# Optimization experiments

Hardware: AMD Instinct MI355X
Metric: run time of the kernel (lower is better)

The kernel has to match this reference:

```python
import jax, jax.numpy as jnp
import numpy as np

H = 2048      # hidden_size
DM = 4096     # intermediate_size
N = 16        # ssm state size
K = 4         # conv kernel
R = 128       # time_step_rank
B_SZ = 1
L = 1024


def setup_inputs() -> dict:
    key = jax.random.key(0)
    ks = jax.random.split(key, 10)
    s = 0.02
    hidden_states = jax.random.normal(ks[0], (B_SZ, L, H), dtype=jnp.float32)
    W_in = jax.random.normal(ks[1], (2 * DM, H), dtype=jnp.float32) * s
    conv_w = jax.random.normal(ks[2], (DM, 1, K), dtype=jnp.float32) * 0.3
    conv_b = jax.random.normal(ks[3], (DM,), dtype=jnp.float32) * 0.1
    W_x = jax.random.normal(ks[4], (R + 2 * N, DM), dtype=jnp.float32) * s
    W_dt = jax.random.normal(ks[5], (DM, R), dtype=jnp.float32) * s
    b_dt = jax.random.normal(ks[6], (DM,), dtype=jnp.float32) * 0.1
    # A_log init: log(arange(1..N)) broadcast over channels (per __init__)
    A_log = jnp.broadcast_to(jnp.log(jnp.arange(1, N + 1, dtype=jnp.float32))[None, :], (DM, N)).copy()
    D_param = jnp.ones((DM,), dtype=jnp.float32)
    W_out = jax.random.normal(ks[7], (H, DM), dtype=jnp.float32) * s
    return {"hidden_states": hidden_states, "W_in": W_in, "conv_w": conv_w,
            "conv_b": conv_b, "W_x": W_x, "W_dt": W_dt, "b_dt": b_dt,
            "A_log": A_log, "D_param": D_param, "W_out": W_out}


def reference(hidden_states, W_in, conv_w, conv_b, W_x, W_dt, b_dt, A_log, D_param, W_out):
    # in_proj then chunk into hidden / gate (torch chunks dim=1 after transpose)
    proj = hidden_states @ W_in.T                     # [B, L, 2D]
    h, gate = proj[..., :DM], proj[..., DM:]          # each [B, L, D]
    # depthwise causal conv1d, padding K-1 then truncate to L (left-pad == same)
    h_cl = jnp.transpose(h, (0, 2, 1))                # [B, D, L]
    hc = jax.lax.conv_general_dilated(
        h_cl, conv_w, window_strides=(1,), padding=[(K - 1, 0)],
        dimension_numbers=("NCH", "OIH", "NCH"), feature_group_count=DM)
    hc = jax.nn.silu(hc + conv_b[None, :, None])      # [B, D, L]
    hc_ld = jnp.transpose(hc, (0, 2, 1))              # [B, L, D]
    # x_proj -> dt, B, C
    ssm_p = hc_ld @ W_x.T                             # [B, L, R+2N]
    ts, Bm, Cm = ssm_p[..., :R], ssm_p[..., R:R + N], ssm_p[..., R + N:]
    dt = jax.nn.softplus(ts @ W_dt.T + b_dt)          # [B, L, D]
    A = -jnp.exp(A_log)                               # [D, N]
    dA = jnp.exp(dt[:, :, :, None] * A[None, None, :, :])            # [B, L, D, N]
    dBu = dt[:, :, :, None] * Bm[:, :, None, :] * hc_ld[:, :, :, None]  # [B, L, D, N]
    # selective scan over time: state = dA*state + dBu; y = <state, C>
    def step(state, inp):
        dA_t, dBu_t, C_t = inp                        # [B,D,N],[B,D,N],[B,N]
        state = dA_t * state + dBu_t
        y = jnp.einsum("bdn,bn->bd", state, C_t)
        return state, y
    init = jnp.zeros((hidden_states.shape[0], DM, N), dtype=hidden_states.dtype)
    _, ys = jax.lax.scan(step, init,
                         (jnp.swapaxes(dA, 0, 1), jnp.swapaxes(dBu, 0, 1), jnp.swapaxes(Cm, 0, 1)))
    y = jnp.transpose(ys, (1, 0, 2))                  # [B, L, D]
    y = y + hc_ld * D_param[None, None, :]            # skip via D
    y = y * jax.nn.silu(gate)                         # gating
    return y @ W_out.T                                # [B, L, H]
```

## Files before the change

kernel.cpp:

```cpp
#include <hip/hip_runtime.h>
#include <math.h>

#define AS1 __attribute__((address_space(1)))
#define AS3 __attribute__((address_space(3)))

typedef __attribute__((ext_vector_type(8))) short short8;
typedef __attribute__((ext_vector_type(4))) float f32x4;

#define WAITV(n) asm volatile("s_waitcnt vmcnt(" #n ")" ::: "memory")
#define BARRIER() asm volatile("s_barrier" ::: "memory")

static __device__ __forceinline__ unsigned short f2bf(float f) {
    unsigned u = __float_as_uint(f);
    unsigned r = (u + 0x7fffu + ((u >> 16) & 1u)) >> 16;
    return (unsigned short)r;
}
static __device__ __forceinline__ float bf2f(unsigned short u) {
    return __uint_as_float(((unsigned)u) << 16);
}

__global__ __launch_bounds__(256) void cvt_f32_bf16(const float* __restrict__ src,
                                                    unsigned short* __restrict__ dst,
                                                    int n4) {
    int i = blockIdx.x * 256 + threadIdx.x;
    int stride = gridDim.x * 256;
    for (; i < n4; i += stride) {
        float4 v = ((const float4*)src)[i];
        ushort4 o;
        o.x = f2bf(v.x); o.y = f2bf(v.y); o.z = f2bf(v.z); o.w = f2bf(v.w);
        ((ushort4*)dst)[i] = o;
    }
}

__global__ __launch_bounds__(256) void cvt_ts(const float* __restrict__ ssmp,
                                              unsigned short* __restrict__ ts) {
    int i = blockIdx.x * 256 + threadIdx.x;
    int t = i >> 5, c4 = (i & 31) * 4;
    float4 v = *(const float4*)&ssmp[t * 160 + c4];
    ushort4 o;
    o.x = f2bf(v.x); o.y = f2bf(v.y); o.z = f2bf(v.z); o.w = f2bf(v.w);
    *(ushort4*)&ts[t * 128 + c4] = o;
}

__global__ __launch_bounds__(256) void conv_silu(const float* __restrict__ h,
                                                 const float* __restrict__ cw,
                                                 const float* __restrict__ cb,
                                                 unsigned short* __restrict__ hc_bf) {
    int idx = blockIdx.x * 256 + threadIdx.x;
    int d = idx & 4095, t = idx >> 12;
    float acc = cb[d];
    float4 w = *(const float4*)&cw[d * 4];
    const float* wp = (const float*)&w;
#pragma unroll
    for (int k = 0; k < 4; ++k) {
        int tt = t + k - 3;
        if (tt >= 0) acc += h[tt * 4096 + d] * wp[k];
    }
    float s = acc / (1.f + __expf(-acc));
    hc_bf[idx] = f2bf(s);
}

__global__ __launch_bounds__(256) void reduce4(const float* __restrict__ pA,
                                               const float* __restrict__ pB,
                                               float* __restrict__ out, int n4) {
    int i = blockIdx.x * 256 + threadIdx.x;
    int stride = gridDim.x * 256;
    const size_t MN4 = (size_t)1024 * 2048 / 4;
    for (; i < n4; i += stride) {
        float4 a = ((const float4*)pA)[i];
        float4 b = ((const float4*)pA)[i + MN4];
        float4 c = ((const float4*)pB)[i];
        float4 d = ((const float4*)pB)[i + MN4];
        float4 o;
        o.x = (a.x + b.x) + (c.x + d.x);
        o.y = (a.y + b.y) + (c.y + d.y);
        o.z = (a.z + b.z) + (c.z + d.z);
        o.w = (a.w + b.w) + (c.w + d.w);
        ((float4*)out)[i] = o;
    }
}

enum { P_GATE = 0, P_PART = 1 };

template <int EPI>
__global__ __launch_bounds__(512, 2)
void gemm8p(const short* __restrict__ A, const short* __restrict__ B,
            void* __restrict__ C0v, void* __restrict__ C1v,
            int N, int K, int kchunk) {
    __shared__ short lds[3 * 24576];

    const int tid = threadIdx.x;
    const int wv = tid >> 6, ln = tid & 63;
    const int lr = ln & 15, kg = ln >> 4;
    const int wm = wv >> 2, wn = wv & 3;

    const int nwg = gridDim.x;
    const int bid = blockIdx.x;
    const int swz = (bid & 7) * (nwg >> 3) + (bid >> 3);
    const int by = swz & 7, bx = swz >> 3;
    const int m0 = by * 128;
    const int n0 = bx * 256;
    const int kbeg = blockIdx.z * kchunk;
    const int NT = kchunk >> 6;

    f32x4 acc[4][4];
#pragma unroll
    for (int mi = 0; mi < 4; ++mi)
#pragma unroll
        for (int ni = 0; ni < 4; ++ni) acc[mi][ni] = (f32x4){0.f, 0.f, 0.f, 0.f};

    const short* Abase = A + (size_t)m0 * K + kbeg;
    const short* Bbase = B + (size_t)n0 * K + kbeg;

#define STAGE(kt, b)                                                          \
    {                                                                         \
        short* lbase = &lds[(b) * 24576];                                     \
        _Pragma("unroll")                                                     \
        for (int r = 0; r < 2; ++r) {                                         \
            int c = r * 512 + tid;                                            \
            int row = c >> 3, cb8 = (c & 7) << 4;                             \
            int scb = cb8 ^ ((row & 7) << 4);                                 \
            const short* src = Abase + (size_t)row * K + (kt) * 64 + (scb >> 1); \
            short* dst = lbase + (r * 512 + wv * 64) * 8;                     \
            __builtin_amdgcn_global_load_lds((const AS1 void*)src,            \
                                             (AS3 void*)dst, 16, 0, 0);       \
        }                                                                     \
        _Pragma("unroll")                                                     \
        for (int r = 0; r < 4; ++r) {                                         \
            int c = r * 512 + tid;                                            \
            int row = c >> 3, cb8 = (c & 7) << 4;                             \
            int scb = cb8 ^ ((row & 7) << 4);                                 \
            const short* src = Bbase + (size_t)row * K + (kt) * 64 + (scb >> 1); \
            short* dst = lbase + 8192 + (r * 512 + wv * 64) * 8;              \
            __builtin_amdgcn_global_load_lds((const AS1 void*)src,            \
                                             (AS3 void*)dst, 16, 0, 0);       \
        }                                                                     \
    }
#define RD_A(dst, mi, ks)                                                     \
    { int row = wm * 64 + (mi) * 16 + lr;                                     \
      int col = ((ks) * 32 + kg * 8) ^ ((row & 7) << 3);                      \
      dst = *(const short8*)&la[row * 64 + col]; }
#define RD_B(dst, ni, ks)                                                     \
    { int row = wn * 64 + (ni) * 16 + lr;                                     \
      int col = ((ks) * 32 + kg * 8) ^ ((row & 7) << 3);                      \
      dst = *(const short8*)&lb[row * 64 + col]; }
#define MFMA4(mi, a)                                                          \
    acc[mi][0] = __builtin_amdgcn_mfma_f32_16x16x32_bf16(a, vb0, acc[mi][0], 0, 0, 0); \
    acc[mi][1] = __builtin_amdgcn_mfma_f32_16x16x32_bf16(a, vb1, acc[mi][1], 0, 0, 0); \
    acc[mi][2] = __builtin_amdgcn_mfma_f32_16x16x32_bf16(a, vb2, acc[mi][2], 0, 0, 0); \
    acc[mi][3] = __builtin_amdgcn_mfma_f32_16x16x32_bf16(a, vb3, acc[mi][3], 0, 0, 0);

    STAGE(0, 0);
    STAGE(1, 1);

    for (int kt = 0; kt < NT; ++kt) {
        const int b = kt % 3;
        if (kt + 1 < NT) { WAITV(6); } else { WAITV(0); }
        BARRIER();
        if (kt + 2 < NT) STAGE(kt + 2, (kt + 2) % 3);

        const short* la = &lds[b * 24576];
        const short* lb = la + 8192;
        short8 va0, va1, va2, va3, vb0, vb1, vb2, vb3;
        RD_B(vb0, 0, 0); RD_B(vb1, 1, 0); RD_B(vb2, 2, 0); RD_B(vb3, 3, 0);
        RD_A(va0, 0, 0); RD_A(va1, 1, 0); RD_A(va2, 2, 0); RD_A(va3, 3, 0);
        __builtin_amdgcn_s_setprio(1);
        MFMA4(0, va0); MFMA4(1, va1); MFMA4(2, va2); MFMA4(3, va3);
        __builtin_amdgcn_s_setprio(0);
        RD_B(vb0, 0, 1); RD_B(vb1, 1, 1); RD_B(vb2, 2, 1); RD_B(vb3, 3, 1);
        RD_A(va0, 0, 1); RD_A(va1, 1, 1); RD_A(va2, 2, 1); RD_A(va3, 3, 1);
        __builtin_amdgcn_s_setprio(1);
        MFMA4(0, va0); MFMA4(1, va1); MFMA4(2, va2); MFMA4(3, va3);
        __builtin_amdgcn_s_setprio(0);
    }
#undef STAGE
#undef RD_A
#undef RD_B
#undef MFMA4

#pragma unroll
    for (int mi = 0; mi < 4; ++mi) {
        int crow0 = m0 + wm * 64 + mi * 16 + kg * 4;
#pragma unroll
        for (int ni = 0; ni < 4; ++ni) {
            int ccol = n0 + wn * 64 + ni * 16 + lr;
#pragma unroll
            for (int i = 0; i < 4; ++i) {
                float v = acc[mi][ni][i];
                size_t crow = (size_t)(crow0 + i);
                if constexpr (EPI == P_GATE) {
                    if (ccol < 4096) ((float*)C0v)[crow * 4096 + ccol] = v;
                    else {
                        float s = v / (1.f + __expf(-v));
                        ((unsigned short*)C1v)[crow * 4096 + (ccol - 4096)] = f2bf(s);
                    }
                } else {
                    float* P = (float*)(blockIdx.z < 2 ? C0v : C1v) +
                               (size_t)(blockIdx.z & 1) * 1024 * 2048;
                    P[crow * N + ccol] = v;
                }
            }
        }
    }
}

enum { EPI_PLAIN = 0, EPI_SPLIT = 1, EPI_ATOMIC = 2, EPI_SOFTPLUS = 3 };

template <int BM, int EPI>
__global__ __launch_bounds__(256)
void gemm_bt(const short* __restrict__ A, const short* __restrict__ B,
             float* __restrict__ C, float* __restrict__ C2,
             const float* __restrict__ bias,
             int M, int N, int K, int ldc, int kcLen) {
    __shared__ short A_lds[BM * 32];
    __shared__ short B_lds[128 * 32];
    const int tid = threadIdx.x;
    const int wv = tid >> 6, ln = tid & 63;
    const int lr = ln & 15, kg = ln >> 4;
    const int m0 = blockIdx.y * BM;
    const int n0 = blockIdx.x * 128;
    const int kbeg = blockIdx.z * kcLen;
    const int kend = kbeg + kcLen;
    const int wm = wv >> 1, wn = wv & 1;
    constexpr int MR = BM / 32;

    f32x4 acc[MR][4];
#pragma unroll
    for (int mi = 0; mi < MR; ++mi)
#pragma unroll
        for (int ni = 0; ni < 4; ++ni) acc[mi][ni] = (f32x4){0.f, 0.f, 0.f, 0.f};

    const int arow = tid >> 2;
    const int kq8 = (tid & 3) * 8;

    for (int k0 = kbeg; k0 < kend; k0 += 32) {
#pragma unroll
        for (int r = 0; r < BM / 64; ++r) {
            const short* srcA = A + (size_t)(m0 + r * 64 + arow) * K + (k0 + kq8);
            short* dstA = &A_lds[(r * 64 + wv * 16) * 32];
            __builtin_amdgcn_global_load_lds((const AS1 void*)srcA, (AS3 void*)dstA, 16, 0, 0);
        }
#pragma unroll
        for (int r = 0; r < 2; ++r) {
            int brow = n0 + r * 64 + arow;
            if (brow > N - 1) brow = N - 1;
            const short* srcB = B + (size_t)brow * K + (k0 + kq8);
            short* dstB = &B_lds[(r * 64 + wv * 16) * 32];
            __builtin_amdgcn_global_load_lds((const AS1 void*)srcB, (AS3 void*)dstB, 16, 0, 0);
        }
        __syncthreads();

        short8 av[MR], bv[4];
#pragma unroll
        for (int mi = 0; mi < MR; ++mi)
            av[mi] = *(const short8*)&A_lds[(wm * (BM / 2) + mi * 16 + lr) * 32 + kg * 8];
#pragma unroll
        for (int ni = 0; ni < 4; ++ni)
            bv[ni] = *(const short8*)&B_lds[(wn * 64 + ni * 16 + lr) * 32 + kg * 8];
#pragma unroll
        for (int mi = 0; mi < MR; ++mi)
#pragma unroll
            for (int ni = 0; ni < 4; ++ni)
                acc[mi][ni] = __builtin_amdgcn_mfma_f32_16x16x32_bf16(av[mi], bv[ni], acc[mi][ni], 0, 0, 0);
        __syncthreads();
    }

#pragma unroll
    for (int mi = 0; mi < MR; ++mi) {
        int crow0 = m0 + wm * (BM / 2) + mi * 16 + kg * 4;
#pragma unroll
        for (int ni = 0; ni < 4; ++ni) {
            int ccol = n0 + wn * 64 + ni * 16 + lr;
#pragma unroll
            for (int i = 0; i < 4; ++i) {
                float v = acc[mi][ni][i];
                size_t crow = (size_t)(crow0 + i);
                if constexpr (EPI == EPI_PLAIN) {
                    C[crow * ldc + ccol] = v;
                } else if constexpr (EPI == EPI_SPLIT) {
                    if (ccol < 4096) C[crow * 4096 + ccol] = v;
                    else C2[crow * 4096 + (ccol - 4096)] = v;
                } else if constexpr (EPI == EPI_ATOMIC) {
                    if (ccol < N) atomicAdd(&C[crow * ldc + ccol], v);
                } else {
                    float x = v + bias[ccol];
                    float sp = fmaxf(x, 0.f) + log1pf(__expf(-fabsf(x)));
                    ((unsigned short*)C)[crow * ldc + ccol] = f2bf(sp);
                }
            }
        }
    }
}

#define CLEN 16
#define NCH 64

__global__ __launch_bounds__(256)
void scan_p1(const unsigned short* __restrict__ dt, const unsigned short* __restrict__ hc,
             const float* __restrict__ ssmp, const float* __restrict__ A_log,
             float* __restrict__ Sbuf, float* __restrict__ dtsum) {
    const int tid = threadIdx.x;
    const int c = blockIdx.x & (NCH - 1);
    const int db = blockIdx.x >> 6;
    const int d = db * 256 + tid;
    const int t0 = c * CLEN;

    float Ac[16];
#pragma unroll
    for (int i = 0; i < 4; ++i) {
        float4 v = *(const float4*)&A_log[d * 16 + i * 4];
        Ac[i*4+0] = -__expf(v.x); Ac[i*4+1] = -__expf(v.y);
        Ac[i*4+2] = -__expf(v.z); Ac[i*4+3] = -__expf(v.w);
    }

    __shared__ float sB[CLEN][16];
    sB[tid >> 4][tid & 15] = ssmp[(t0 + (tid >> 4)) * 160 + 128 + (tid & 15)];
    __syncthreads();

    float st[16];
#pragma unroll
    for (int n = 0; n < 16; ++n) st[n] = 0.f;
    float ds = 0.f;

    for (int tt = 0; tt < CLEN; ++tt) {
        size_t g = (size_t)(t0 + tt) * 4096 + d;
        float dtv = bf2f(dt[g]);
        float hcv = bf2f(hc[g]);
        float du = dtv * hcv;
        ds += dtv;
#pragma unroll
        for (int n = 0; n < 16; ++n) {
            float dA = __expf(dtv * Ac[n]);
            st[n] = fmaf(dA, st[n], du * sB[tt][n]);
        }
    }

    float* o = Sbuf + ((size_t)c * 4096 + d) * 16;
#pragma unroll
    for (int i = 0; i < 4; ++i)
        *(float4*)&o[i * 4] = make_float4(st[i*4], st[i*4+1], st[i*4+2], st[i*4+3]);
    dtsum[c * 4096 + d] = ds;
}

__global__ __launch_bounds__(256)
void scan_p2(const float* __restrict__ A_log, const float* __restrict__ dtsum,
             float* __restrict__ S) {
    const int idx = blockIdx.x * 256 + threadIdx.x;
    const int d = idx >> 4;
    const float Ac = -__expf(A_log[idx]);

    float sl[NCH], Pv[NCH];
#pragma unroll
    for (int c = 0; c < NCH; ++c) sl[c] = S[(size_t)c * 65536 + idx];
#pragma unroll
    for (int c = 0; c < NCH; ++c) Pv[c] = __expf(Ac * dtsum[c * 4096 + d]);

    float s = 0.f;
#pragma unroll
    for (int c = 0; c < NCH; ++c) {
        S[(size_t)c * 65536 + idx] = s;
        s = fmaf(Pv[c], s, sl[c]);
    }
}

__global__ __launch_bounds__(256)
void scan_p3(const unsigned short* __restrict__ dt, const unsigned short* __restrict__ hc,
             const float* __restrict__ ssmp, const float* __restrict__ A_log,
             const float* __restrict__ Dp, const unsigned short* __restrict__ gate,
             const float* __restrict__ Sinit, unsigned short* __restrict__ y_bf) {
    const int tid = threadIdx.x;
    const int c = blockIdx.x & (NCH - 1);
    const int db = blockIdx.x >> 6;
    const int d = db * 256 + tid;
    const int t0 = c * CLEN;

    float Ac[16];
#pragma unroll
    for (int i = 0; i < 4; ++i) {
        float4 v = *(const float4*)&A_log[d * 16 + i * 4];
        Ac[i*4+0] = -__expf(v.x); Ac[i*4+1] = -__expf(v.y);
        Ac[i*4+2] = -__expf(v.z); Ac[i*4+3] = -__expf(v.w);
    }
    const float Dcoef = Dp[d];

    __shared__ float sB[CLEN][16], sC[CLEN][16];
    {
        int tt = tid >> 4, nn = tid & 15;
        sB[tt][nn] = ssmp[(t0 + tt) * 160 + 128 + nn];
        sC[tt][nn] = ssmp[(t0 + tt) * 160 + 144 + nn];
    }
    __syncthreads();

    float st[16];
    {
        const float* si = Sinit + ((size_t)c * 4096 + d) * 16;
#pragma unroll
        for (int i = 0; i < 4; ++i) {
            float4 v = *(const float4*)&si[i * 4];
            st[i*4] = v.x; st[i*4+1] = v.y; st[i*4+2] = v.z; st[i*4+3] = v.w;
        }
    }

    for (int tt = 0; tt < CLEN; ++tt) {
        size_t g = (size_t)(t0 + tt) * 4096 + d;
        float dtv = bf2f(dt[g]);
        float hcv = bf2f(hc[g]);
        float du = dtv * hcv;
        float p[16];
#pragma unroll
        for (int n = 0; n < 16; ++n) {
            float dA = __expf(dtv * Ac[n]);
            st[n] = fmaf(dA, st[n], du * sB[tt][n]);
            p[n] = st[n] * sC[tt][n];
        }
#pragma unroll
        for (int n = 0; n < 8; ++n) p[n] += p[n + 8];
#pragma unroll
        for (int n = 0; n < 4; ++n) p[n] += p[n + 4];
        p[0] += p[2]; p[1] += p[3];
        float csum = p[0] + p[1];
        float gv = bf2f(gate[g]);
        float yv = (csum + hcv * Dcoef) * gv;
        y_bf[g] = f2bf(yv);
    }
}

extern "C" void kernel_launch(void* const* d_in, const int* in_sizes, int n_in,
                              void* d_out, int out_size, void* d_ws, size_t ws_size,
                              hipStream_t stream) {
    (void)in_sizes; (void)n_in; (void)out_size; (void)ws_size;
    const float* hidden = (const float*)d_in[0];
    const float* W_in   = (const float*)d_in[1];
    const float* conv_w = (const float*)d_in[2];
    const float* conv_b = (const float*)d_in[3];
    const float* W_x    = (const float*)d_in[4];
    const float* W_dt   = (const float*)d_in[5];
    const float* b_dt   = (const float*)d_in[6];
    const float* A_log  = (const float*)d_in[7];
    const float* D_p    = (const float*)d_in[8];
    const float* W_out  = (const float*)d_in[9];
    float* out = (float*)d_out;

    char* w = (char*)d_ws;
    unsigned short* hid_bf = (unsigned short*)w;  w += (size_t)1024 * 2048 * 2;
    unsigned short* Wbig   = (unsigned short*)w;  w += (size_t)8192 * 2048 * 2;
    float* h_buf           = (float*)w;           w += (size_t)1024 * 4096 * 4;
    unsigned short* gate_bf= (unsigned short*)w;  w += (size_t)1024 * 4096 * 2;
    unsigned short* hc_bf  = (unsigned short*)w;  w += (size_t)1024 * 4096 * 2;
    unsigned short* dt_bf  = (unsigned short*)w;  w += (size_t)1024 * 4096 * 2;
    float* ssmp            = (float*)w;           w += (size_t)1024 * 160 * 4;
    unsigned short* ts_bf  = (unsigned short*)w;  w += (size_t)1024 * 128 * 2;
    unsigned short* Wx_bf  = (unsigned short*)w;  w += (size_t)160 * 4096 * 2;
    unsigned short* Wdt_bf = (unsigned short*)w;  w += (size_t)4096 * 128 * 2;
    unsigned short* y_bf   = (unsigned short*)w;  w += (size_t)1024 * 4096 * 2;
    float* Sbuf            = (float*)w;           w += (size_t)NCH * 4096 * 16 * 4;
    float* dtsum           = (float*)w;           w += (size_t)NCH * 4096 * 4;

    hipMemsetAsync(ssmp, 0, (size_t)1024 * 160 * 4, stream);

    cvt_f32_bf16<<<2048, 256, 0, stream>>>(hidden, hid_bf, 1024 * 2048 / 4);
    cvt_f32_bf16<<<4096, 256, 0, stream>>>(W_in, Wbig, 8192 * 2048 / 4);
    cvt_f32_bf16<<<640, 256, 0, stream>>>(W_x, Wx_bf, 160 * 4096 / 4);
    cvt_f32_bf16<<<512, 256, 0, stream>>>(W_dt, Wdt_bf, 4096 * 128 / 4);

    gemm8p<P_GATE><<<dim3(256, 1, 1), 512, 0, stream>>>(
        (const short*)hid_bf, (const short*)Wbig, h_buf, gate_bf, 8192, 2048, 2048);

    conv_silu<<<16384, 256, 0, stream>>>(h_buf, conv_w, conv_b, hc_bf);

    cvt_f32_bf16<<<2048, 256, 0, stream>>>(W_out, Wbig, 2048 * 4096 / 4);

    gemm_bt<128, EPI_ATOMIC><<<dim3(2, 8, 16), 256, 0, stream>>>(
        (const short*)hc_bf, (const short*)Wx_bf, ssmp, nullptr, nullptr,
        1024, 160, 4096, 160, 256);

    cvt_ts<<<128, 256, 0, stream>>>(ssmp, ts_bf);

    gemm_bt<128, EPI_SOFTPLUS><<<dim3(32, 8, 1), 256, 0, stream>>>(
        (const short*)ts_bf, (const short*)Wdt_bf, (float*)dt_bf, nullptr, b_dt,
        1024, 4096, 128, 4096, 128);

    scan_p1<<<NCH * 16, 256, 0, stream>>>(dt_bf, hc_bf, ssmp, A_log, Sbuf, dtsum);
    scan_p2<<<256, 256, 0, stream>>>(A_log, dtsum, Sbuf);
    scan_p3<<<NCH * 16, 256, 0, stream>>>(dt_bf, hc_bf, ssmp, A_log, D_p, gate_bf, Sbuf, y_bf);

    gemm8p<P_PART><<<dim3(64, 1, 4), 512, 0, stream>>>(
        (const short*)y_bf, (const short*)Wbig, Sbuf, h_buf, 2048, 4096, 1024);
    reduce4<<<2048, 256, 0, stream>>>(Sbuf, h_buf, out, 1024 * 2048 / 4);
}
```

Before: 216.1 us.

## Use 4-wave 64x128 warp tiles in gemm8p and store h as bf16

The 128x256 GEMM block now runs on 4 waves instead of 8. Each wave computes a 64x128 sub-tile with 32 accumulators, and the vmcnt waits are rescaled for the larger per-thread staging loads. The goal is more MFMA work per LDS fragment read and fewer waves contending for each block. Separately, the in_proj epilogue writes the h half as bf16 instead of fp32, and conv_silu reads bf16, which halves that intermediate's traffic at some precision cost. The larger accumulator set raises register pressure, and the block now has half as many waves to hide latency.

```diff
diff --git a/kernel.cpp b/kernel.cpp
--- a/kernel.cpp
+++ b/kernel.cpp
@@ -42,7 +42,7 @@
     *(ushort4*)&ts[t * 128 + c4] = o;
 }
 
-__global__ __launch_bounds__(256) void conv_silu(const float* __restrict__ h,
+__global__ __launch_bounds__(256) void conv_silu(const unsigned short* __restrict__ h,
                                                  const float* __restrict__ cw,
                                                  const float* __restrict__ cb,
                                                  unsigned short* __restrict__ hc_bf) {
@@ -54,7 +54,7 @@
 #pragma unroll
     for (int k = 0; k < 4; ++k) {
         int tt = t + k - 3;
-        if (tt >= 0) acc += h[tt * 4096 + d] * wp[k];
+        if (tt >= 0) acc += bf2f(h[tt * 4096 + d]) * wp[k];
     }
     float s = acc / (1.f + __expf(-acc));
     hc_bf[idx] = f2bf(s);
@@ -83,7 +83,7 @@
 enum { P_GATE = 0, P_PART = 1 };
 
 template <int EPI>
-__global__ __launch_bounds__(512, 2)
+__global__ __launch_bounds__(256, 1)
 void gemm8p(const short* __restrict__ A, const short* __restrict__ B,
             void* __restrict__ C0v, void* __restrict__ C1v,
             int N, int K, int kchunk) {
@@ -92,7 +92,7 @@
     const int tid = threadIdx.x;
     const int wv = tid >> 6, ln = tid & 63;
     const int lr = ln & 15, kg = ln >> 4;
-    const int wm = wv >> 2, wn = wv & 3;
+    const int wm = wv >> 1, wn = wv & 1;
 
     const int nwg = gridDim.x;
     const int bid = blockIdx.x;
@@ -103,11 +103,11 @@
     const int kbeg = blockIdx.z * kchunk;
     const int NT = kchunk >> 6;
 
-    f32x4 acc[4][4];
+    f32x4 acc[4][8];
 #pragma unroll
     for (int mi = 0; mi < 4; ++mi)
 #pragma unroll
-        for (int ni = 0; ni < 4; ++ni) acc[mi][ni] = (f32x4){0.f, 0.f, 0.f, 0.f};
+        for (int ni = 0; ni < 8; ++ni) acc[mi][ni] = (f32x4){0.f, 0.f, 0.f, 0.f};
 
     const short* Abase = A + (size_t)m0 * K + kbeg;
     const short* Bbase = B + (size_t)n0 * K + kbeg;
@@ -116,22 +116,22 @@
     {                                                                         \
         short* lbase = &lds[(b) * 24576];                                     \
         _Pragma("unroll")                                                     \
-        for (int r = 0; r < 2; ++r) {                                         \
-            int c = r * 512 + tid;                                            \
+        for (int r = 0; r < 4; ++r) {                                         \
+            int c = r * 256 + tid;                                            \
             int row = c >> 3, cb8 = (c & 7) << 4;                             \
             int scb = cb8 ^ ((row & 7) << 4);                                 \
             const short* src = Abase + (size_t)row * K + (kt) * 64 + (scb >> 1); \
-            short* dst = lbase + (r * 512 + wv * 64) * 8;                     \
+            short* dst = lbase + (r * 256 + wv * 64) * 8;                     \
             __builtin_amdgcn_global_load_lds((const AS1 void*)src,            \
                                              (AS3 void*)dst, 16, 0, 0);       \
         }                                                                     \
         _Pragma("unroll")                                                     \
-        for (int r = 0; r < 4; ++r) {                                         \
-            int c = r * 512 + tid;                                            \
+        for (int r = 0; r < 8; ++r) {                                         \
+            int c = r * 256 + tid;                                            \
             int row = c >> 3, cb8 = (c & 7) << 4;                             \
             int scb = cb8 ^ ((row & 7) << 4);                                 \
             const short* src = Bbase + (size_t)row * K + (kt) * 64 + (scb >> 1); \
-            short* dst = lbase + 8192 + (r * 512 + wv * 64) * 8;              \
+            short* dst = lbase + 8192 + (r * 256 + wv * 64) * 8;              \
             __builtin_amdgcn_global_load_lds((const AS1 void*)src,            \
                                              (AS3 void*)dst, 16, 0, 0);       \
         }                                                                     \
@@ -141,55 +141,63 @@
       int col = ((ks) * 32 + kg * 8) ^ ((row & 7) << 3);                      \
       dst = *(const short8*)&la[row * 64 + col]; }
 #define RD_B(dst, ni, ks)                                                     \
-    { int row = wn * 64 + (ni) * 16 + lr;                                     \
+    { int row = wn * 128 + (ni) * 16 + lr;                                    \
       int col = ((ks) * 32 + kg * 8) ^ ((row & 7) << 3);                      \
       dst = *(const short8*)&lb[row * 64 + col]; }
-#define MFMA4(mi, a)                                                          \
+#define MFMA8(mi, a)                                                          \
     acc[mi][0] = __builtin_amdgcn_mfma_f32_16x16x32_bf16(a, vb0, acc[mi][0], 0, 0, 0); \
     acc[mi][1] = __builtin_amdgcn_mfma_f32_16x16x32_bf16(a, vb1, acc[mi][1], 0, 0, 0); \
     acc[mi][2] = __builtin_amdgcn_mfma_f32_16x16x32_bf16(a, vb2, acc[mi][2], 0, 0, 0); \
-    acc[mi][3] = __builtin_amdgcn_mfma_f32_16x16x32_bf16(a, vb3, acc[mi][3], 0, 0, 0);
+    acc[mi][3] = __builtin_amdgcn_mfma_f32_16x16x32_bf16(a, vb3, acc[mi][3], 0, 0, 0); \
+    acc[mi][4] = __builtin_amdgcn_mfma_f32_16x16x32_bf16(a, vb4, acc[mi][4], 0, 0, 0); \
+    acc[mi][5] = __builtin_amdgcn_mfma_f32_16x16x32_bf16(a, vb5, acc[mi][5], 0, 0, 0); \
+    acc[mi][6] = __builtin_amdgcn_mfma_f32_16x16x32_bf16(a, vb6, acc[mi][6], 0, 0, 0); \
+    acc[mi][7] = __builtin_amdgcn_mfma_f32_16x16x32_bf16(a, vb7, acc[mi][7], 0, 0, 0);
 
     STAGE(0, 0);
     STAGE(1, 1);
 
     for (int kt = 0; kt < NT; ++kt) {
         const int b = kt % 3;
-        if (kt + 1 < NT) { WAITV(6); } else { WAITV(0); }
+        int ahead = NT - 1 - kt;
+        if (ahead > 2) ahead = 2;
+        if (ahead == 2) { WAITV(24); } else if (ahead == 1) { WAITV(12); } else { WAITV(0); }
         BARRIER();
         if (kt + 2 < NT) STAGE(kt + 2, (kt + 2) % 3);
 
         const short* la = &lds[b * 24576];
         const short* lb = la + 8192;
-        short8 va0, va1, va2, va3, vb0, vb1, vb2, vb3;
+        short8 va0, va1, va2, va3, vb0, vb1, vb2, vb3, vb4, vb5, vb6, vb7;
         RD_B(vb0, 0, 0); RD_B(vb1, 1, 0); RD_B(vb2, 2, 0); RD_B(vb3, 3, 0);
+        RD_B(vb4, 4, 0); RD_B(vb5, 5, 0); RD_B(vb6, 6, 0); RD_B(vb7, 7, 0);
         RD_A(va0, 0, 0); RD_A(va1, 1, 0); RD_A(va2, 2, 0); RD_A(va3, 3, 0);
         __builtin_amdgcn_s_setprio(1);
-        MFMA4(0, va0); MFMA4(1, va1); MFMA4(2, va2); MFMA4(3, va3);
+        MFMA8(0, va0); MFMA8(1, va1); MFMA8(2, va2); MFMA8(3, va3);
         __builtin_amdgcn_s_setprio(0);
         RD_B(vb0, 0, 1); RD_B(vb1, 1, 1); RD_B(vb2, 2, 1); RD_B(vb3, 3, 1);
+        RD_B(vb4, 4, 1); RD_B(vb5, 5, 1); RD_B(vb6, 6, 1); RD_B(vb7, 7, 1);
         RD_A(va0, 0, 1); RD_A(va1, 1, 1); RD_A(va2, 2, 1); RD_A(va3, 3, 1);
         __builtin_amdgcn_s_setprio(1);
-        MFMA4(0, va0); MFMA4(1, va1); MFMA4(2, va2); MFMA4(3, va3);
+        MFMA8(0, va0); MFMA8(1, va1); MFMA8(2, va2); MFMA8(3, va3);
         __builtin_amdgcn_s_setprio(0);
     }
 #undef STAGE
 #undef RD_A
 #undef RD_B
-#undef MFMA4
+#undef MFMA8
 
 #pragma unroll
     for (int mi = 0; mi < 4; ++mi) {
         int crow0 = m0 + wm * 64 + mi * 16 + kg * 4;
 #pragma unroll
-        for (int ni = 0; ni < 4; ++ni) {
-            int ccol = n0 + wn * 64 + ni * 16 + lr;
+        for (int ni = 0; ni < 8; ++ni) {
+            int ccol = n0 + wn * 128 + ni * 16 + lr;
 #pragma unroll
             for (int i = 0; i < 4; ++i) {
                 float v = acc[mi][ni][i];
                 size_t crow = (size_t)(crow0 + i);
                 if constexpr (EPI == P_GATE) {
-                    if (ccol < 4096) ((float*)C0v)[crow * 4096 + ccol] = v;
+                    if (ccol < 4096) ((unsigned short*)C0v)[crow * 4096 + ccol] = f2bf(v);
                     else {
                         float s = v / (1.f + __expf(-v));
                         ((unsigned short*)C1v)[crow * 4096 + (ccol - 4096)] = f2bf(s);
@@ -463,10 +471,10 @@
     cvt_f32_bf16<<<640, 256, 0, stream>>>(W_x, Wx_bf, 160 * 4096 / 4);
     cvt_f32_bf16<<<512, 256, 0, stream>>>(W_dt, Wdt_bf, 4096 * 128 / 4);
 
-    gemm8p<P_GATE><<<dim3(256, 1, 1), 512, 0, stream>>>(
+    gemm8p<P_GATE><<<dim3(256, 1, 1), 256, 0, stream>>>(
         (const short*)hid_bf, (const short*)Wbig, h_buf, gate_bf, 8192, 2048, 2048);
 
-    conv_silu<<<16384, 256, 0, stream>>>(h_buf, conv_w, conv_b, hc_bf);
+    conv_silu<<<16384, 256, 0, stream>>>((const unsigned short*)h_buf, conv_w, conv_b, hc_bf);
 
     cvt_f32_bf16<<<2048, 256, 0, stream>>>(W_out, Wbig, 2048 * 4096 / 4);
 
@@ -484,7 +492,7 @@
     scan_p2<<<256, 256, 0, stream>>>(A_log, dtsum, Sbuf);
     scan_p3<<<NCH * 16, 256, 0, stream>>>(dt_bf, hc_bf, ssmp, A_log, D_p, gate_bf, Sbuf, y_bf);
 
-    gemm8p<P_PART><<<dim3(64, 1, 4), 512, 0, stream>>>(
+    gemm8p<P_PART><<<dim3(64, 1, 4), 256, 0, stream>>>(
         (const short*)y_bf, (const short*)Wbig, Sbuf, h_buf, 2048, 4096, 1024);
     reduce4<<<2048, 256, 0, stream>>>(Sbuf, h_buf, out, 1024 * 2048 / 4);
 }
```

After: 231.9 us. +7.3%, slower.

## Use 256x256 split-K GEMM tiles with bf16 partials and fused reduce epilogues

Applied to the files above, without the earlier changes.

Replaces the 128x256 GEMM with a 256x256 tile kernel that uses a K-step of 32, staggers its A and B staging across two barriers, and writes bf16 partial sums. The in-projection becomes split-K by 2, with a reduce kernel that sums the partials, applies SiLU to the gate half and stores h in bf16. The output projection becomes split-K by 8, reduced to fp32. The intent is higher MFMA reuse per tile and less traffic for partials and for h. The cost is extra reduce passes, a workspace buffer aliased across stages, and some loss of precision from rounding partials to bf16.

```diff
diff --git a/kernel.cpp b/kernel.cpp
--- a/kernel.cpp
+++ b/kernel.cpp
@@ -5,6 +5,7 @@
 #define AS3 __attribute__((address_space(3)))
 
 typedef __attribute__((ext_vector_type(8))) short short8;
+typedef __attribute__((ext_vector_type(8))) unsigned short ushort8_t;
 typedef __attribute__((ext_vector_type(4))) float f32x4;
 
 #define WAITV(n) asm volatile("s_waitcnt vmcnt(" #n ")" ::: "memory")
@@ -42,7 +43,7 @@
     *(ushort4*)&ts[t * 128 + c4] = o;
 }
 
-__global__ __launch_bounds__(256) void conv_silu(const float* __restrict__ h,
+__global__ __launch_bounds__(256) void conv_silu(const unsigned short* __restrict__ h,
                                                  const float* __restrict__ cw,
                                                  const float* __restrict__ cb,
                                                  unsigned short* __restrict__ hc_bf) {
@@ -54,40 +55,60 @@
 #pragma unroll
     for (int k = 0; k < 4; ++k) {
         int tt = t + k - 3;
-        if (tt >= 0) acc += h[tt * 4096 + d] * wp[k];
+        if (tt >= 0) acc += bf2f(h[tt * 4096 + d]) * wp[k];
     }
     float s = acc / (1.f + __expf(-acc));
     hc_bf[idx] = f2bf(s);
 }
 
-__global__ __launch_bounds__(256) void reduce4(const float* __restrict__ pA,
-                                               const float* __restrict__ pB,
-                                               float* __restrict__ out, int n4) {
+__global__ __launch_bounds__(256) void reduce2(const unsigned short* __restrict__ P,
+                                               unsigned short* __restrict__ h_bf,
+                                               unsigned short* __restrict__ gate_bf) {
+    const int NCHK = 1024 * 8192 / 8;
     int i = blockIdx.x * 256 + threadIdx.x;
     int stride = gridDim.x * 256;
-    const size_t MN4 = (size_t)1024 * 2048 / 4;
-    for (; i < n4; i += stride) {
-        float4 a = ((const float4*)pA)[i];
-        float4 b = ((const float4*)pA)[i + MN4];
-        float4 c = ((const float4*)pB)[i];
-        float4 d = ((const float4*)pB)[i + MN4];
-        float4 o;
-        o.x = (a.x + b.x) + (c.x + d.x);
-        o.y = (a.y + b.y) + (c.y + d.y);
-        o.z = (a.z + b.z) + (c.z + d.z);
-        o.w = (a.w + b.w) + (c.w + d.w);
-        ((float4*)out)[i] = o;
-    }
-}
-
-enum { P_GATE = 0, P_PART = 1 };
-
-template <int EPI>
+    for (; i < NCHK; i += stride) {
+        ushort8_t a = ((const ushort8_t*)P)[i];
+        ushort8_t b = ((const ushort8_t*)P)[i + NCHK];
+        int e0 = i * 8;
+        int row = e0 >> 13, col = e0 & 8191;
+        ushort8_t o;
+        if (col < 4096) {
+#pragma unroll
+            for (int j = 0; j < 8; ++j) o[j] = f2bf(bf2f(a[j]) + bf2f(b[j]));
+            ((ushort8_t*)h_bf)[(row * 4096 + col) >> 3] = o;
+        } else {
+#pragma unroll
+            for (int j = 0; j < 8; ++j) {
+                float v = bf2f(a[j]) + bf2f(b[j]);
+                o[j] = f2bf(v / (1.f + __expf(-v)));
+            }
+            ((ushort8_t*)gate_bf)[(row * 4096 + (col - 4096)) >> 3] = o;
+        }
+    }
+}
+
+__global__ __launch_bounds__(256) void reduce8(const unsigned short* __restrict__ P,
+                                               float* __restrict__ out) {
+    const int NCHK = 1024 * 2048 / 4;
+    int i = blockIdx.x * 256 + threadIdx.x;
+    int stride = gridDim.x * 256;
+    for (; i < NCHK; i += stride) {
+        float4 s = make_float4(0.f, 0.f, 0.f, 0.f);
+#pragma unroll
+        for (int z = 0; z < 8; ++z) {
+            ushort4 v = ((const ushort4*)(P + (size_t)z * 1024 * 2048))[i];
+            s.x += bf2f(v.x); s.y += bf2f(v.y); s.z += bf2f(v.z); s.w += bf2f(v.w);
+        }
+        ((float4*)out)[i] = s;
+    }
+}
+
 __global__ __launch_bounds__(512, 2)
-void gemm8p(const short* __restrict__ A, const short* __restrict__ B,
-            void* __restrict__ C0v, void* __restrict__ C1v,
-            int N, int K, int kchunk) {
-    __shared__ short lds[3 * 24576];
+void gemm256p(const short* __restrict__ A, const short* __restrict__ B,
+              unsigned short* __restrict__ Pbase,
+              int N, int K, int kchunk) {
+    __shared__ short lds[3 * 16384];
 
     const int tid = threadIdx.x;
     const int wv = tid >> 6, ln = tid & 63;
@@ -97,109 +118,86 @@
     const int nwg = gridDim.x;
     const int bid = blockIdx.x;
     const int swz = (bid & 7) * (nwg >> 3) + (bid >> 3);
-    const int by = swz & 7, bx = swz >> 3;
-    const int m0 = by * 128;
-    const int n0 = bx * 256;
+    const int by = swz & 3, bx = swz >> 2;
+    const int m0 = by * 256, n0 = bx * 256;
     const int kbeg = blockIdx.z * kchunk;
-    const int NT = kchunk >> 6;
-
-    f32x4 acc[4][4];
-#pragma unroll
-    for (int mi = 0; mi < 4; ++mi)
+    const int NT = kchunk >> 5;
+
+    f32x4 acc[8][4];
+#pragma unroll
+    for (int mi = 0; mi < 8; ++mi)
 #pragma unroll
         for (int ni = 0; ni < 4; ++ni) acc[mi][ni] = (f32x4){0.f, 0.f, 0.f, 0.f};
 
     const short* Abase = A + (size_t)m0 * K + kbeg;
     const short* Bbase = B + (size_t)n0 * K + kbeg;
 
-#define STAGE(kt, b)                                                          \
+#define STG(gbase, ldsoff, kt, b, pass)                                       \
     {                                                                         \
-        short* lbase = &lds[(b) * 24576];                                     \
-        _Pragma("unroll")                                                     \
-        for (int r = 0; r < 2; ++r) {                                         \
-            int c = r * 512 + tid;                                            \
-            int row = c >> 3, cb8 = (c & 7) << 4;                             \
-            int scb = cb8 ^ ((row & 7) << 4);                                 \
-            const short* src = Abase + (size_t)row * K + (kt) * 64 + (scb >> 1); \
-            short* dst = lbase + (r * 512 + wv * 64) * 8;                     \
-            __builtin_amdgcn_global_load_lds((const AS1 void*)src,            \
-                                             (AS3 void*)dst, 16, 0, 0);       \
-        }                                                                     \
-        _Pragma("unroll")                                                     \
-        for (int r = 0; r < 4; ++r) {                                         \
-            int c = r * 512 + tid;                                            \
-            int row = c >> 3, cb8 = (c & 7) << 4;                             \
-            int scb = cb8 ^ ((row & 7) << 4);                                 \
-            const short* src = Bbase + (size_t)row * K + (kt) * 64 + (scb >> 1); \
-            short* dst = lbase + 8192 + (r * 512 + wv * 64) * 8;              \
-            __builtin_amdgcn_global_load_lds((const AS1 void*)src,            \
-                                             (AS3 void*)dst, 16, 0, 0);       \
-        }                                                                     \
-    }
-#define RD_A(dst, mi, ks)                                                     \
-    { int row = wm * 64 + (mi) * 16 + lr;                                     \
-      int col = ((ks) * 32 + kg * 8) ^ ((row & 7) << 3);                      \
-      dst = *(const short8*)&la[row * 64 + col]; }
-#define RD_B(dst, ni, ks)                                                     \
+        int c = (pass) * 512 + tid;                                           \
+        int row = c >> 2, ch = (c & 3) * 8;                                   \
+        const short* src = (gbase) + (size_t)row * K + (kt) * 32 + ch;        \
+        short* dst = &lds[(b) * 16384 + (ldsoff) + ((pass) * 512 + wv * 64) * 8]; \
+        __builtin_amdgcn_global_load_lds((const AS1 void*)src,                \
+                                         (AS3 void*)dst, 16, 0, 0);           \
+    }
+#define STAGE_A(kt, b) { STG(Abase, 0, kt, b, 0); STG(Abase, 0, kt, b, 1); }
+#define STAGE_B(kt, b) { STG(Bbase, 8192, kt, b, 0); STG(Bbase, 8192, kt, b, 1); }
+#define RD_A(dst, mi)                                                         \
+    { int row = wm * 128 + (mi) * 16 + lr;                                    \
+      dst = *(const short8*)&la[row * 32 + kg * 8]; }
+#define RD_B(dst, ni)                                                         \
     { int row = wn * 64 + (ni) * 16 + lr;                                     \
-      int col = ((ks) * 32 + kg * 8) ^ ((row & 7) << 3);                      \
-      dst = *(const short8*)&lb[row * 64 + col]; }
+      dst = *(const short8*)&lb[row * 32 + kg * 8]; }
 #define MFMA4(mi, a)                                                          \
     acc[mi][0] = __builtin_amdgcn_mfma_f32_16x16x32_bf16(a, vb0, acc[mi][0], 0, 0, 0); \
     acc[mi][1] = __builtin_amdgcn_mfma_f32_16x16x32_bf16(a, vb1, acc[mi][1], 0, 0, 0); \
     acc[mi][2] = __builtin_amdgcn_mfma_f32_16x16x32_bf16(a, vb2, acc[mi][2], 0, 0, 0); \
     acc[mi][3] = __builtin_amdgcn_mfma_f32_16x16x32_bf16(a, vb3, acc[mi][3], 0, 0, 0);
 
-    STAGE(0, 0);
-    STAGE(1, 1);
-
+    STAGE_A(0, 0); STAGE_B(0, 0);
+    STAGE_A(1, 1); STAGE_B(1, 1);
+
+    int b = 0;
     for (int kt = 0; kt < NT; ++kt) {
-        const int b = kt % 3;
-        if (kt + 1 < NT) { WAITV(6); } else { WAITV(0); }
+        if (kt + 1 < NT) { WAITV(4); } else { WAITV(0); }
         BARRIER();
-        if (kt + 2 < NT) STAGE(kt + 2, (kt + 2) % 3);
-
-        const short* la = &lds[b * 24576];
+        int bn = b + 2; if (bn >= 3) bn -= 3;
+        if (kt + 2 < NT) STAGE_A(kt + 2, bn);
+
+        const short* la = &lds[b * 16384];
         const short* lb = la + 8192;
         short8 va0, va1, va2, va3, vb0, vb1, vb2, vb3;
-        RD_B(vb0, 0, 0); RD_B(vb1, 1, 0); RD_B(vb2, 2, 0); RD_B(vb3, 3, 0);
-        RD_A(va0, 0, 0); RD_A(va1, 1, 0); RD_A(va2, 2, 0); RD_A(va3, 3, 0);
+        RD_B(vb0, 0); RD_B(vb1, 1); RD_B(vb2, 2); RD_B(vb3, 3);
+        RD_A(va0, 0); RD_A(va1, 1); RD_A(va2, 2); RD_A(va3, 3);
         __builtin_amdgcn_s_setprio(1);
         MFMA4(0, va0); MFMA4(1, va1); MFMA4(2, va2); MFMA4(3, va3);
         __builtin_amdgcn_s_setprio(0);
-        RD_B(vb0, 0, 1); RD_B(vb1, 1, 1); RD_B(vb2, 2, 1); RD_B(vb3, 3, 1);
-        RD_A(va0, 0, 1); RD_A(va1, 1, 1); RD_A(va2, 2, 1); RD_A(va3, 3, 1);
+        BARRIER();
+        if (kt + 2 < NT) STAGE_B(kt + 2, bn);
+        RD_A(va0, 4); RD_A(va1, 5); RD_A(va2, 6); RD_A(va3, 7);
         __builtin_amdgcn_s_setprio(1);
-        MFMA4(0, va0); MFMA4(1, va1); MFMA4(2, va2); MFMA4(3, va3);
+        MFMA4(4, va0); MFMA4(5, va1); MFMA4(6, va2); MFMA4(7, va3);
         __builtin_amdgcn_s_setprio(0);
-    }
-#undef STAGE
+        b = (b + 1 == 3) ? 0 : b + 1;
+    }
+#undef STG
+#undef STAGE_A
+#undef STAGE_B
 #undef RD_A
 #undef RD_B
 #undef MFMA4
 
-#pragma unroll
-    for (int mi = 0; mi < 4; ++mi) {
-        int crow0 = m0 + wm * 64 + mi * 16 + kg * 4;
+    unsigned short* P = Pbase + (size_t)blockIdx.z * 1024 * N;
+#pragma unroll
+    for (int mi = 0; mi < 8; ++mi) {
+        int crow0 = m0 + wm * 128 + mi * 16 + kg * 4;
 #pragma unroll
         for (int ni = 0; ni < 4; ++ni) {
             int ccol = n0 + wn * 64 + ni * 16 + lr;
 #pragma unroll
-            for (int i = 0; i < 4; ++i) {
-                float v = acc[mi][ni][i];
-                size_t crow = (size_t)(crow0 + i);
-                if constexpr (EPI == P_GATE) {
-                    if (ccol < 4096) ((float*)C0v)[crow * 4096 + ccol] = v;
-                    else {
-                        float s = v / (1.f + __expf(-v));
-                        ((unsigned short*)C1v)[crow * 4096 + (ccol - 4096)] = f2bf(s);
-                    }
-                } else {
-                    float* P = (float*)(blockIdx.z < 2 ? C0v : C1v) +
-                               (size_t)(blockIdx.z & 1) * 1024 * 2048;
-                    P[crow * N + ccol] = v;
-                }
-            }
+            for (int i = 0; i < 4; ++i)
+                P[(size_t)(crow0 + i) * N + ccol] = f2bf(acc[mi][ni][i]);
         }
     }
 }
@@ -444,16 +442,17 @@
     char* w = (char*)d_ws;
     unsigned short* hid_bf = (unsigned short*)w;  w += (size_t)1024 * 2048 * 2;
     unsigned short* Wbig   = (unsigned short*)w;  w += (size_t)8192 * 2048 * 2;
-    float* h_buf           = (float*)w;           w += (size_t)1024 * 4096 * 4;
+    unsigned short* h_bf   = (unsigned short*)w;  w += (size_t)1024 * 4096 * 2;
     unsigned short* gate_bf= (unsigned short*)w;  w += (size_t)1024 * 4096 * 2;
-    unsigned short* hc_bf  = (unsigned short*)w;  w += (size_t)1024 * 4096 * 2;
-    unsigned short* dt_bf  = (unsigned short*)w;  w += (size_t)1024 * 4096 * 2;
+    unsigned short* pscr   = (unsigned short*)w;  w += (size_t)16 * 1024 * 1024 * 2;
+    unsigned short* hc_bf  = pscr;
+    unsigned short* dt_bf  = pscr + (size_t)1024 * 4096;
+    float* Sbuf            = (float*)(pscr + (size_t)2 * 1024 * 4096);
     float* ssmp            = (float*)w;           w += (size_t)1024 * 160 * 4;
     unsigned short* ts_bf  = (unsigned short*)w;  w += (size_t)1024 * 128 * 2;
     unsigned short* Wx_bf  = (unsigned short*)w;  w += (size_t)160 * 4096 * 2;
     unsigned short* Wdt_bf = (unsigned short*)w;  w += (size_t)4096 * 128 * 2;
     unsigned short* y_bf   = (unsigned short*)w;  w += (size_t)1024 * 4096 * 2;
-    float* Sbuf            = (float*)w;           w += (size_t)NCH * 4096 * 16 * 4;
     float* dtsum           = (float*)w;           w += (size_t)NCH * 4096 * 4;
 
     hipMemsetAsync(ssmp, 0, (size_t)1024 * 160 * 4, stream);
@@ -463,10 +462,11 @@
     cvt_f32_bf16<<<640, 256, 0, stream>>>(W_x, Wx_bf, 160 * 4096 / 4);
     cvt_f32_bf16<<<512, 256, 0, stream>>>(W_dt, Wdt_bf, 4096 * 128 / 4);
 
-    gemm8p<P_GATE><<<dim3(256, 1, 1), 512, 0, stream>>>(
-        (const short*)hid_bf, (const short*)Wbig, h_buf, gate_bf, 8192, 2048, 2048);
-
-    conv_silu<<<16384, 256, 0, stream>>>(h_buf, conv_w, conv_b, hc_bf);
+    gemm256p<<<dim3(128, 1, 2), 512, 0, stream>>>(
+        (const short*)hid_bf, (const short*)Wbig, pscr, 8192, 2048, 1024);
+    reduce2<<<2048, 256, 0, stream>>>(pscr, h_bf, gate_bf);
+
+    conv_silu<<<16384, 256, 0, stream>>>(h_bf, conv_w, conv_b, hc_bf);
 
     cvt_f32_bf16<<<2048, 256, 0, stream>>>(W_out, Wbig, 2048 * 4096 / 4);
 
@@ -484,7 +484,7 @@
     scan_p2<<<256, 256, 0, stream>>>(A_log, dtsum, Sbuf);
     scan_p3<<<NCH * 16, 256, 0, stream>>>(dt_bf, hc_bf, ssmp, A_log, D_p, gate_bf, Sbuf, y_bf);
 
-    gemm8p<P_PART><<<dim3(64, 1, 4), 512, 0, stream>>>(
-        (const short*)y_bf, (const short*)Wbig, Sbuf, h_buf, 2048, 4096, 1024);
-    reduce4<<<2048, 256, 0, stream>>>(Sbuf, h_buf, out, 1024 * 2048 / 4);
-}
+    gemm256p<<<dim3(32, 1, 8), 512, 0, stream>>>(
+        (const short*)y_bf, (const short*)Wbig, pscr, 2048, 4096, 512);
+    reduce8<<<2048, 256, 0, stream>>>(pscr, out);
+}
```

Measured after the change: 227.8 us. 5.4% more time.
